# Kernel tuning notes

Measured on AMD Instinct MI355X. Metric: run time of the kernel, lower is better.

Reference implementation:

```python
import jax, jax.numpy as jnp
import numpy as np

B, N, C = 4, 1024, 1024
H = 16
HD = C // H
FF = 4 * C
EPS = 1e-6


def layernorm(x, g, b):
    mu = jnp.mean(x, axis=-1, keepdims=True)
    var = jnp.mean((x - mu) ** 2, axis=-1, keepdims=True)
    return (x - mu) * jax.lax.rsqrt(var + EPS) * g + b


def setup_inputs() -> dict:
    key = jax.random.key(0)
    ks = jax.random.split(key, 16)
    s = lambda fan_in: 1.0 / np.sqrt(fan_in)
    inp = {
        "x": jax.random.normal(ks[0], (B, N, C), dtype=jnp.float32),
        "qkv_w": jax.random.normal(ks[1], (3 * C, C), dtype=jnp.float32) * s(C),
        "qkv_b": jnp.zeros((3 * C,), jnp.float32),
        "attn_proj_w": jax.random.normal(ks[2], (C, C), dtype=jnp.float32) * s(C),
        "attn_proj_b": jnp.zeros((C,), jnp.float32),
        "blk_proj_w": jax.random.normal(ks[3], (C, C), dtype=jnp.float32) * s(C),
        "blk_proj_b": jnp.zeros((C,), jnp.float32),
        "ln1_g": jnp.ones((C,), jnp.float32),
        "ln1_b": jnp.zeros((C,), jnp.float32),
        "ln2_g": jnp.ones((C,), jnp.float32),
        "ln2_b": jnp.zeros((C,), jnp.float32),
        "fc1_w": jax.random.normal(ks[4], (FF, C), dtype=jnp.float32) * s(C),
        "fc1_b": jnp.zeros((FF,), jnp.float32),
        "fc2_w": jax.random.normal(ks[5], (C, FF), dtype=jnp.float32) * s(FF),
        "fc2_b": jnp.zeros((C,), jnp.float32),
        "mask": jnp.ones((B, N), jnp.int32),  # unused by the original forward
    }
    return inp


def reference(x, qkv_w, qkv_b, attn_proj_w, attn_proj_b, blk_proj_w, blk_proj_b,
              ln1_g, ln1_b, ln2_g, ln2_b, fc1_w, fc1_b, fc2_w, fc2_b, mask):
    shortcut = x
    xn = layernorm(x, ln1_g, ln1_b)

    # QKV projection: [B,N,3C] -> [3,B,H,N,HD]
    qkv = xn @ qkv_w.T + qkv_b
    qkv = qkv.reshape(B, N, 3, H, HD).transpose(2, 0, 3, 1, 4)
    q, k, v = qkv[0], qkv[1], qkv[2]
    scale = HD ** -0.5
    attn = jnp.einsum('bhqd,bhkd->bhqk', q * scale, k)
    attn = jax.nn.softmax(attn, axis=-1)
    o = jnp.einsum('bhqk,bhkd->bhqd', attn, v)
    o = o.transpose(0, 2, 1, 3).reshape(B, N, C)
    o = o @ attn_proj_w.T + attn_proj_b  # attention-internal proj

    x = shortcut + (o @ blk_proj_w.T + blk_proj_b)  # Block's extra proj + residual

    h = layernorm(x, ln2_g, ln2_b)
    h = jax.nn.gelu(h @ fc1_w.T + fc1_b, approximate=False)
    h = h @ fc2_w.T + fc2_b
    return x + h
```

## Files before the change

### kernel.cpp

```cpp
#include <hip/hip_runtime.h>

typedef unsigned short u16;
typedef __attribute__((ext_vector_type(8))) short short8;
typedef __attribute__((ext_vector_type(4))) float f32x4;

#define DEVI __device__ __forceinline__

static constexpr int Nn = 1024;
static constexpr int Cc = 1024;

DEVI u16 f2bf(float f) {
  union { float f; unsigned u; } v; v.f = f;
  unsigned r = v.u + 0x7fffu + ((v.u >> 16) & 1u);
  return (u16)(r >> 16);
}

DEVI void async_ld16(const void* g, void* lds) {
  __builtin_amdgcn_global_load_lds(
      (__attribute__((address_space(1))) void*)g,
      (__attribute__((address_space(3))) void*)lds, 16, 0, 0);
}

__global__ __launch_bounds__(256) void cvt_all(
    const float* __restrict__ s0, const float* __restrict__ s2,
    const float* __restrict__ s3, const float* __restrict__ s4,
    u16* __restrict__ out) {
  const size_t j = ((size_t)blockIdx.x * 256 + threadIdx.x) * 4;
  size_t i; const float* src; size_t lo;
  if (j < 3145728) { i = j; src = s0; lo = 0; }
  else {
    i = j + 1048576;
    if (i < 5242880)      { src = s2; lo = 4194304; }
    else if (i < 9437184) { src = s3; lo = 5242880; }
    else                  { src = s4; lo = 9437184; }
  }
  const float4 v = *(const float4*)&src[i - lo];
  ushort4 o;
  o.x = f2bf(v.x); o.y = f2bf(v.y); o.z = f2bf(v.z); o.w = f2bf(v.w);
  *(ushort4*)&out[i] = o;
}

__global__ __launch_bounds__(256) void transpose_wT(const float* __restrict__ in,
                                                    u16* __restrict__ out) {
  __shared__ u16 tile[64][72];
  const int bx = blockIdx.x & 15, by = blockIdx.x >> 4;
  const int tr = threadIdx.x >> 2;
  const int tc4 = (threadIdx.x & 3) * 16;
#pragma unroll
  for (int j = 0; j < 4; ++j) {
    const float4 v = *(const float4*)&in[(size_t)(by * 64 + tr) * 1024 +
                                         bx * 64 + tc4 + j * 4];
    tile[tc4 + j * 4 + 0][tr] = f2bf(v.x);
    tile[tc4 + j * 4 + 1][tr] = f2bf(v.y);
    tile[tc4 + j * 4 + 2][tr] = f2bf(v.z);
    tile[tc4 + j * 4 + 3][tr] = f2bf(v.w);
  }
  __syncthreads();
#pragma unroll
  for (int j = 0; j < 4; ++j) {
    ushort4 o;
    o.x = tile[tr][tc4 + j * 4 + 0];
    o.y = tile[tr][tc4 + j * 4 + 1];
    o.z = tile[tr][tc4 + j * 4 + 2];
    o.w = tile[tr][tc4 + j * 4 + 3];
    *(ushort4*)&out[(size_t)(bx * 64 + tr) * 1024 + by * 64 + tc4 + j * 4] = o;
  }
}

__global__ __launch_bounds__(256) void cbias_k(const float* __restrict__ apb,
                                               const float* __restrict__ bpw,
                                               const float* __restrict__ bpb,
                                               float* __restrict__ cb) {
  const int j = blockIdx.x * 4 + (threadIdx.x >> 6);
  const int lane = threadIdx.x & 63;
  float s = 0.f;
  for (int k = lane; k < 1024; k += 64) s += apb[k] * bpw[(size_t)j * 1024 + k];
#pragma unroll
  for (int m = 1; m < 64; m <<= 1) s += __shfl_xor(s, m);
  if (lane == 0) cb[j] = s + bpb[j];
}

__global__ __launch_bounds__(256) void gemm64(const u16* __restrict__ A,
                                              const u16* __restrict__ W,
                                              u16* __restrict__ out, int K) {
  __shared__ __align__(16) u16 As[64 * 64];
  __shared__ __align__(16) u16 Bs[64 * 64];
  const int tid = threadIdx.x;
  const int wave = tid >> 6, lane = tid & 63;
  const int g = lane >> 4, lr = lane & 15;
  const int brow = (blockIdx.x >> 4) << 6, bcol = (blockIdx.x & 15) << 6;
  const int srow = lane >> 3;
  const int scg = (lane & 7) ^ srow;
  const int swz = (lr & 7) << 4;

  f32x4 acc[4];
#pragma unroll
  for (int j = 0; j < 4; ++j) acc[j] = (f32x4){0.f, 0.f, 0.f, 0.f};

  for (int k0 = 0; k0 < K; k0 += 64) {
#pragma unroll
    for (int u = 0; u < 2; ++u) {
      async_ld16(A + (size_t)(brow + u * 32 + wave * 8 + srow) * K + k0 + scg * 8,
                 (char*)As + u * 4096 + wave * 1024);
      async_ld16(W + (size_t)(bcol + u * 32 + wave * 8 + srow) * K + k0 + scg * 8,
                 (char*)Bs + u * 4096 + wave * 1024);
    }
    __syncthreads();
    short8 af[2], bf[4][2];
#pragma unroll
    for (int kk = 0; kk < 2; ++kk)
      af[kk] = *(const short8*)((char*)As + (wave * 16 + lr) * 128 +
                                ((kk * 64 + g * 16) ^ swz));
#pragma unroll
    for (int nf = 0; nf < 4; ++nf)
#pragma unroll
      for (int kk = 0; kk < 2; ++kk)
        bf[nf][kk] = *(const short8*)((char*)Bs + (nf * 16 + lr) * 128 +
                                      ((kk * 64 + g * 16) ^ swz));
#pragma unroll
    for (int kk = 0; kk < 2; ++kk)
#pragma unroll
      for (int nf = 0; nf < 4; ++nf)
        acc[nf] = __builtin_amdgcn_mfma_f32_16x16x32_bf16(af[kk], bf[nf][kk],
                                                          acc[nf], 0, 0, 0);
    __syncthreads();
  }
#pragma unroll
  for (int nf = 0; nf < 4; ++nf)
#pragma unroll
    for (int reg = 0; reg < 4; ++reg)
      out[(size_t)(brow + wave * 16 + g * 4 + reg) * 1024 +
          bcol + nf * 16 + lr] = f2bf(acc[nf][reg]);
}

__global__ __launch_bounds__(256) void vtrans(const u16* __restrict__ qkv,
                                              u16* __restrict__ vt) {
  __shared__ u16 tile[64][72];
  const int bh = blockIdx.x >> 4, tb = blockIdx.x & 15;
  const int b = bh >> 4, h = bh & 15;
  const int t0 = tb * 64;
  const int tid = threadIdx.x;
  const int rr = tid >> 3, c8 = (tid & 7) * 8;
#pragma unroll
  for (int r = 0; r < 2; ++r) {
    const int t = r * 32 + rr;
    const short8 v = *(const short8*)(qkv + (size_t)(b * Nn + t0 + t) * 3072 +
                                      2048 + h * 64 + c8);
#pragma unroll
    for (int j = 0; j < 8; ++j) tile[t][c8 + j] = (u16)v[j];
  }
  __syncthreads();
#pragma unroll
  for (int r = 0; r < 2; ++r) {
    const int d = r * 32 + rr;
    short8 o;
#pragma unroll
    for (int j = 0; j < 8; ++j) o[j] = (short)tile[c8 + j][d];
    *(short8*)(vt + (size_t)(bh * 64 + d) * 1024 + t0 + c8) = o;
  }
}

__global__ __launch_bounds__(256) void ln_bf16(const float* __restrict__ x,
                                               const float* __restrict__ gg,
                                               const float* __restrict__ bb,
                                               u16* __restrict__ out) {
  const int row = blockIdx.x;
  const float4 v = ((const float4*)(x + (size_t)row * 1024))[threadIdx.x];
  float s  = v.x + v.y + v.z + v.w;
  float s2 = v.x * v.x + v.y * v.y + v.z * v.z + v.w * v.w;
#pragma unroll
  for (int m = 1; m < 64; m <<= 1) { s += __shfl_xor(s, m); s2 += __shfl_xor(s2, m); }
  __shared__ float ps[4], ps2[4];
  const int wave = threadIdx.x >> 6;
  if ((threadIdx.x & 63) == 0) { ps[wave] = s; ps2[wave] = s2; }
  __syncthreads();
  s = ps[0] + ps[1] + ps[2] + ps[3];
  s2 = ps2[0] + ps2[1] + ps2[2] + ps2[3];
  const float mu = s * (1.0f / 1024.0f);
  const float var = s2 * (1.0f / 1024.0f) - mu * mu;
  const float rs = rsqrtf(var + 1e-6f);
  const float4 gv = ((const float4*)gg)[threadIdx.x];
  const float4 bv = ((const float4*)bb)[threadIdx.x];
  ushort4 o;
  o.x = f2bf((v.x - mu) * rs * gv.x + bv.x);
  o.y = f2bf((v.y - mu) * rs * gv.y + bv.y);
  o.z = f2bf((v.z - mu) * rs * gv.z + bv.z);
  o.w = f2bf((v.w - mu) * rs * gv.w + bv.w);
  ((ushort4*)(out + (size_t)row * 1024))[threadIdx.x] = o;
}

template <bool GELU_, bool OUTBF>
__global__ __launch_bounds__(512, 4) void gemmS(
    const u16* __restrict__ A, const u16* __restrict__ W,
    const float* __restrict__ bias, void* __restrict__ out,
    int M, int N, int K) {
  __shared__ __align__(16) u16 As[256 * 64];
  __shared__ __align__(16) u16 Bs[128 * 64];
  const int tid = threadIdx.x;
  const int wave = tid >> 6, lane = tid & 63;
  const int g = lane >> 4, lr = lane & 15;
  const int wm = wave >> 1, wn = wave & 1;
  const int ntile = N >> 7;
  const int nwg = gridDim.x;
  int bid = blockIdx.x;
  bid = (bid & 7) * (nwg >> 3) + (bid >> 3);
  const int brow = (bid / ntile) << 8, bcol = (bid % ntile) << 7;

  const int sru = wave * 8 + (lane >> 3);
  const int scg = (lane & 7) ^ (lane >> 3);
  const int swz = (lr & 7) << 4;

  f32x4 acc[4][4];
#pragma unroll
  for (int i = 0; i < 4; ++i)
#pragma unroll
    for (int j = 0; j < 4; ++j) acc[i][j] = (f32x4){0.f, 0.f, 0.f, 0.f};

  for (int k0 = 0; k0 < K; k0 += 64) {
#pragma unroll
    for (int u = 0; u < 2; ++u)
      async_ld16(W + (size_t)(bcol + u * 64 + sru) * K + k0 + scg * 8,
                 (char*)Bs + u * 8192 + wave * 1024);
#pragma unroll
    for (int u = 0; u < 4; ++u)
      async_ld16(A + (size_t)(brow + u * 64 + sru) * K + k0 + scg * 8,
                 (char*)As + u * 8192 + wave * 1024);
    asm volatile("s_waitcnt vmcnt(0)" ::: "memory");
    __builtin_amdgcn_s_barrier();

    short8 bf[4][2];
#pragma unroll
    for (int nf = 0; nf < 4; ++nf) {
      const int row = wn * 64 + nf * 16 + lr;
#pragma unroll
      for (int kk = 0; kk < 2; ++kk)
        bf[nf][kk] = *(const short8*)((const char*)Bs + row * 128 +
                                      ((kk * 64 + g * 16) ^ swz));
    }
    __builtin_amdgcn_s_setprio(1);
#pragma unroll
    for (int mf = 0; mf < 4; ++mf) {
      short8 af[2];
      const int row = wm * 64 + mf * 16 + lr;
#pragma unroll
      for (int kk = 0; kk < 2; ++kk)
        af[kk] = *(const short8*)((const char*)As + row * 128 +
                                  ((kk * 64 + g * 16) ^ swz));
#pragma unroll
      for (int nf = 0; nf < 4; ++nf)
#pragma unroll
        for (int kk = 0; kk < 2; ++kk)
          acc[mf][nf] = __builtin_amdgcn_mfma_f32_16x16x32_bf16(
              af[kk], bf[nf][kk], acc[mf][nf], 0, 0, 0);
    }
    __builtin_amdgcn_s_setprio(0);
    __builtin_amdgcn_s_barrier();
  }

#pragma unroll
  for (int mf = 0; mf < 4; ++mf)
#pragma unroll
    for (int nf = 0; nf < 4; ++nf) {
      const int cI = bcol + wn * 64 + nf * 16 + lr;
      const float bv = bias[cI];
#pragma unroll
      for (int reg = 0; reg < 4; ++reg) {
        const int r = brow + wm * 64 + mf * 16 + g * 4 + reg;
        float v = acc[mf][nf][reg] + bv;
        if (GELU_) v = 0.5f * v * (1.0f + erff(v * 0.70710678118654752f));
        if (OUTBF) ((u16*)out)[(size_t)r * N + cI] = f2bf(v);
        else       ((float*)out)[(size_t)r * N + cI] = v;
      }
    }
}

template <bool RESID, bool OUTBF>
__global__ __launch_bounds__(512, 2) void gemm128t(
    const u16* __restrict__ A, const u16* __restrict__ W,
    const float* __restrict__ bias, const float* __restrict__ resid,
    void* __restrict__ out, int M, int N, int K) {
  __shared__ __align__(16) u16 smem[49152];
  const int tid = threadIdx.x;
  const int wave = tid >> 6, lane = tid & 63;
  const int g = lane >> 4, lr = lane & 15;
  const int kg = wave & 1, ws = wave >> 1;
  const int wm = ws >> 1, wn = ws & 1;
  const int ntile = N >> 7;
  const int nwg = gridDim.x;
  int bid = blockIdx.x;
  bid = (bid & 7) * (nwg >> 3) + (bid >> 3);
  const int brow = (bid / ntile) << 7, bcol = (bid % ntile) << 7;

  const int sru = wave * 8 + (lane >> 3);
  const int scg = (lane & 7) ^ (lane >> 3);
  const int NT = K >> 6;

  f32x4 acc[4][4];
#pragma unroll
  for (int i = 0; i < 4; ++i)
#pragma unroll
    for (int j = 0; j < 4; ++j) acc[i][j] = (f32x4){0.f, 0.f, 0.f, 0.f};

  auto STAGE = [&](int b, int kt) {
    char* base = (char*)smem + b * 32768;
#pragma unroll
    for (int u = 0; u < 2; ++u)
      async_ld16(W + (size_t)(bcol + u * 64 + sru) * K + (size_t)kt * 64 + scg * 8,
                 base + 16384 + u * 8192 + wave * 1024);
#pragma unroll
    for (int u = 0; u < 2; ++u)
      async_ld16(A + (size_t)(brow + u * 64 + sru) * K + (size_t)kt * 64 + scg * 8,
                 base + u * 8192 + wave * 1024);
  };

  const int colb = kg * 64 + g * 16;
  const int swz = (lr & 7) << 4;

  STAGE(0, 0);
  STAGE(1, 1 < NT ? 1 : 0);
  asm volatile("s_waitcnt vmcnt(4)" ::: "memory");
  __builtin_amdgcn_s_barrier();

  for (int t = 0; t < NT; ++t) {
    const int b = t % 3;
    const char* Ab = (const char*)smem + b * 32768;
    const char* Bb = Ab + 16384;

    short8 bf[4], af[4];
#pragma unroll
    for (int nf = 0; nf < 4; ++nf)
      bf[nf] = *(const short8*)(Bb + (wn * 64 + nf * 16 + lr) * 128 +
                                (colb ^ swz));
#pragma unroll
    for (int mf = 0; mf < 2; ++mf) {
      af[mf]     = *(const short8*)(Ab + (wm * 32 + mf * 16 + lr) * 128 +
                                    (colb ^ swz));
      af[mf + 2] = *(const short8*)(Ab + (64 + wm * 32 + mf * 16 + lr) * 128 +
                                    (colb ^ swz));
    }
    {
      const int pt = (t + 2 < NT) ? t + 2 : NT - 1;
      STAGE((t + 2) % 3, pt);
    }
    __builtin_amdgcn_s_setprio(1);
#pragma unroll
    for (int mf = 0; mf < 4; ++mf)
#pragma unroll
      for (int nf = 0; nf < 4; ++nf)
        acc[mf][nf] = __builtin_amdgcn_mfma_f32_16x16x32_bf16(
            af[mf], bf[nf], acc[mf][nf], 0, 0, 0);
    __builtin_amdgcn_s_setprio(0);
    asm volatile("s_waitcnt vmcnt(4)" ::: "memory");
    __builtin_amdgcn_s_barrier();
  }

  asm volatile("s_waitcnt vmcnt(0)" ::: "memory");
  __syncthreads();
  float* pr = (float*)smem + (size_t)((wm << 1) | wn) * 4096;
  if (kg == 1) {
#pragma unroll
    for (int mf = 0; mf < 4; ++mf)
#pragma unroll
      for (int nf = 0; nf < 4; ++nf)
#pragma unroll
        for (int reg = 0; reg < 4; ++reg) {
          const int lrow = mf * 16 + g * 4 + reg;
          const int w = lrow * 64 +
                        ((nf * 16 + lr) ^ (g << 2) ^ ((g & 1) << 4));
          pr[w] = acc[mf][nf][reg];
        }
  }
  __syncthreads();
  if (kg == 0) {
#pragma unroll
    for (int mf = 0; mf < 4; ++mf) {
      const int rb = brow + ((mf < 2) ? wm * 32 + mf * 16
                                      : 64 + wm * 32 + (mf - 2) * 16);
#pragma unroll
      for (int nf = 0; nf < 4; ++nf) {
        const int cI = bcol + wn * 64 + nf * 16 + lr;
        const float bv = bias[cI];
#pragma unroll
        for (int reg = 0; reg < 4; ++reg) {
          const int lrow = mf * 16 + g * 4 + reg;
          const int w = lrow * 64 +
                        ((nf * 16 + lr) ^ (g << 2) ^ ((g & 1) << 4));
          const int r = rb + g * 4 + reg;
          float v = acc[mf][nf][reg] + pr[w] + bv;
          if (RESID) v += resid[(size_t)r * N + cI];
          if (OUTBF) ((u16*)out)[(size_t)r * N + cI] = f2bf(v);
          else       ((float*)out)[(size_t)r * N + cI] = v;
        }
      }
    }
  }
}

__global__ __launch_bounds__(256) void attn_kernel(const u16* __restrict__ qkv,
                                                   const u16* __restrict__ vt,
                                                   u16* __restrict__ o_out) {
  const int D = blockIdx.x;
  const int bh = (D & 7) + 8 * (D >> 7);
  const int qb = (D >> 3) & 15;
  const int b = bh >> 4, h = bh & 15;
  const int tid = threadIdx.x, wave = tid >> 6, lane = tid & 63;
  const int g = lane >> 4, lr = lane & 15;
  const u16* qg = qkv + (size_t)b * Nn * 3072 + h * 64;
  const u16* kg = qg + 1024;
  const u16* vgt = vt + (size_t)bh * 64 * 1024;

  __shared__ __align__(16) u16 Kl[64 * 64];
  __shared__ __align__(16) u16 Vt[64 * 64];
  __shared__ __align__(16) u16 Pl[64 * 64];

  const int q0 = qb * 64 + wave * 16;
  short8 qf[2];
#pragma unroll
  for (int kf = 0; kf < 2; ++kf)
    qf[kf] = *(const short8*)(qg + (size_t)(q0 + lr) * 3072 + kf * 32 + g * 8);

  f32x4 o[4];
  float ll[4];
#pragma unroll
  for (int df = 0; df < 4; ++df) o[df] = (f32x4){0.f, 0.f, 0.f, 0.f};
#pragma unroll
  for (int r = 0; r < 4; ++r) ll[r] = 0.f;

  for (int t0 = 0; t0 < Nn; t0 += 64) {
#pragma unroll
    for (int r = 0; r < 2; ++r) {
      const int c = r * 256 + wave * 64 + lane;
      const int t = c >> 3;
      const int ob = ((c & 7) << 4) ^ ((t & 7) << 4);
      async_ld16(kg + (size_t)(t0 + t) * 3072 + (ob >> 1),
                 (char*)Kl + (size_t)(r * 256 + wave * 64) * 16);
      async_ld16(vgt + (size_t)t * 1024 + t0 + (ob >> 1),
                 (char*)Vt + (size_t)(r * 256 + wave * 64) * 16);
    }
    __syncthreads();

    short8 kfr[4][2];
#pragma unroll
    for (int tf = 0; tf < 4; ++tf) {
      const int t = tf * 16 + lr;
#pragma unroll
      for (int kf = 0; kf < 2; ++kf)
        kfr[tf][kf] = *(const short8*)((const char*)Kl + t * 128 +
                                       ((kf * 64 + g * 16) ^ ((t & 7) << 4)));
    }
    f32x4 s[4];
    __builtin_amdgcn_s_setprio(1);
#pragma unroll
    for (int tf = 0; tf < 4; ++tf) {
      f32x4 z = (f32x4){0.f, 0.f, 0.f, 0.f};
      z = __builtin_amdgcn_mfma_f32_16x16x32_bf16(qf[0], kfr[tf][0], z, 0, 0, 0);
      z = __builtin_amdgcn_mfma_f32_16x16x32_bf16(qf[1], kfr[tf][1], z, 0, 0, 0);
      s[tf] = z;
    }
    __builtin_amdgcn_s_setprio(0);

    short8 vfr[4][2];
#pragma unroll
    for (int df = 0; df < 4; ++df) {
      const int d = df * 16 + lr;
#pragma unroll
      for (int kf = 0; kf < 2; ++kf)
        vfr[df][kf] = *(const short8*)((const char*)Vt + d * 128 +
                                       ((kf * 64 + g * 16) ^ ((d & 7) << 4)));
    }

#pragma unroll
    for (int tf = 0; tf < 4; ++tf)
#pragma unroll
      for (int reg = 0; reg < 4; ++reg) {
        const float p = __expf(s[tf][reg] * 0.125f);
        s[tf][reg] = p;
        ll[reg] += p;
      }

#pragma unroll
    for (int tf = 0; tf < 4; ++tf)
#pragma unroll
      for (int reg = 0; reg < 4; ++reg) {
        const int m = wave * 16 + g * 4 + reg;
        const int t2 = (tf * 16 + lr) * 2;
        *(u16*)((char*)Pl + m * 128 + (t2 ^ ((m & 7) << 4))) = f2bf(s[tf][reg]);
      }
    short8 pa[2];
#pragma unroll
    for (int kf = 0; kf < 2; ++kf)
      pa[kf] = *(const short8*)((const char*)Pl + (wave * 16 + lr) * 128 +
                                ((kf * 64 + g * 16) ^ ((lr & 7) << 4)));
    __builtin_amdgcn_s_setprio(1);
#pragma unroll
    for (int df = 0; df < 4; ++df) {
      o[df] = __builtin_amdgcn_mfma_f32_16x16x32_bf16(pa[0], vfr[df][0], o[df], 0, 0, 0);
      o[df] = __builtin_amdgcn_mfma_f32_16x16x32_bf16(pa[1], vfr[df][1], o[df], 0, 0, 0);
    }
    __builtin_amdgcn_s_setprio(0);
    __syncthreads();
  }

#pragma unroll
  for (int reg = 0; reg < 4; ++reg) {
#pragma unroll
    for (int msk = 1; msk < 16; msk <<= 1) ll[reg] += __shfl_xor(ll[reg], msk);
    const float inv = 1.0f / ll[reg];
    const int row = b * Nn + qb * 64 + wave * 16 + g * 4 + reg;
#pragma unroll
    for (int df = 0; df < 4; ++df) {
      const int col = h * 64 + df * 16 + lr;
      o_out[(size_t)row * 1024 + col] = f2bf(o[df][reg] * inv);
    }
  }
}

extern "C" void kernel_launch(void* const* d_in, const int* in_sizes, int n_in,
                              void* d_out, int out_size, void* d_ws, size_t ws_size,
                              hipStream_t stream) {
  const float* x    = (const float*)d_in[0];
  const float* qkvw = (const float*)d_in[1];
  const float* qkvb = (const float*)d_in[2];
  const float* apw  = (const float*)d_in[3];
  const float* apb  = (const float*)d_in[4];
  const float* bpw  = (const float*)d_in[5];
  const float* bpb  = (const float*)d_in[6];
  const float* ln1g = (const float*)d_in[7];
  const float* ln1b = (const float*)d_in[8];
  const float* ln2g = (const float*)d_in[9];
  const float* ln2b = (const float*)d_in[10];
  const float* fc1w = (const float*)d_in[11];
  const float* fc1b = (const float*)d_in[12];
  const float* fc2w = (const float*)d_in[13];
  const float* fc2b = (const float*)d_in[14];
  float* out = (float*)d_out;

  char* ws = (char*)d_ws;
  size_t off = 0;
  auto alloc = [&](size_t bytes) {
    char* p = ws + off;
    off += (bytes + 255) & ~(size_t)255;
    return p;
  };
  u16* wqkv  = (u16*)alloc((size_t)3145728 * 2);
  u16* wap   = (u16*)alloc((size_t)1048576 * 2);
  u16* wbp   = (u16*)alloc((size_t)1048576 * 2);
  u16* wfc1  = (u16*)alloc((size_t)4194304 * 2);
  u16* wfc2  = (u16*)alloc((size_t)4194304 * 2);
  u16* xn    = (u16*)alloc((size_t)4194304 * 2);
  u16* qkvbf = (u16*)alloc((size_t)12582912 * 2);
  u16* obuf  = (u16*)alloc((size_t)4194304 * 2);
  float* x2  = (float*)alloc((size_t)4194304 * 4);
  u16* wapT  = (u16*)alloc((size_t)1048576 * 2);
  u16* wc    = (u16*)alloc((size_t)1048576 * 2);
  float* cb  = (float*)alloc(1024 * 4);
  u16* vt    = (u16*)alloc((size_t)4194304 * 2);
  u16* ff    = qkvbf;
  (void)wap;

  cvt_all<<<12288, 256, 0, stream>>>(qkvw, bpw, fc1w, fc2w, wqkv);
  transpose_wT<<<256, 256, 0, stream>>>(apw, wapT);
  cbias_k<<<256, 256, 0, stream>>>(apb, bpw, bpb, cb);

  gemm64<<<256, 256, 0, stream>>>(wbp, wapT, wc, 1024);

  ln_bf16<<<4096, 256, 0, stream>>>(x, ln1g, ln1b, xn);

  gemmS<false, true><<<384, 512, 0, stream>>>(
      xn, wqkv, qkvb, qkvbf, 4096, 3072, 1024);

  vtrans<<<1024, 256, 0, stream>>>(qkvbf, vt);

  attn_kernel<<<1024, 256, 0, stream>>>(qkvbf, vt, obuf);

  gemm128t<true, false><<<256, 512, 0, stream>>>(
      obuf, wc, cb, x, x2, 4096, 1024, 1024);

  ln_bf16<<<4096, 256, 0, stream>>>(x2, ln2g, ln2b, xn);

  gemmS<true, true><<<512, 512, 0, stream>>>(
      xn, wfc1, fc1b, ff, 4096, 4096, 1024);

  gemm128t<true, false><<<256, 512, 0, stream>>>(
      ff, wfc2, fc2b, x2, out, 4096, 1024, 4096);
}
```

Baseline: 226.5 us.

## Triple-buffer K/V tiles in attention kernel with async prefetch two ahead

The attention kernel now keeps three LDS buffers for K and V tiles and issues the async global-to-LDS loads two iterations ahead. A vmcnt wait plus a raw barrier replaces the per-iteration __syncthreads, so loads overlap with the MFMA and softmax work instead of stalling on each tile. A GELU template parameter is added to gemm128t but is disabled at every call site. The extra buffers raise LDS use per block, which may lower occupancy, and the hand-written waitcnt counts must match the number of outstanding loads.

```diff
diff --git a/kernel.cpp b/kernel.cpp
--- a/kernel.cpp
+++ b/kernel.cpp
@@ -274,7 +274,7 @@
     }
 }
 
-template <bool RESID, bool OUTBF>
+template <bool GELU_, bool RESID, bool OUTBF>
 __global__ __launch_bounds__(512, 2) void gemm128t(
     const u16* __restrict__ A, const u16* __restrict__ W,
     const float* __restrict__ bias, const float* __restrict__ resid,
@@ -387,6 +387,7 @@
                         ((nf * 16 + lr) ^ (g << 2) ^ ((g & 1) << 4));
           const int r = rb + g * 4 + reg;
           float v = acc[mf][nf][reg] + pr[w] + bv;
+          if (GELU_) v = 0.5f * v * (1.0f + erff(v * 0.70710678118654752f));
           if (RESID) v += resid[(size_t)r * N + cI];
           if (OUTBF) ((u16*)out)[(size_t)r * N + cI] = f2bf(v);
           else       ((float*)out)[(size_t)r * N + cI] = v;
@@ -409,8 +410,8 @@
   const u16* kg = qg + 1024;
   const u16* vgt = vt + (size_t)bh * 64 * 1024;
 
-  __shared__ __align__(16) u16 Kl[64 * 64];
-  __shared__ __align__(16) u16 Vt[64 * 64];
+  __shared__ __align__(16) u16 Kl[3][64 * 64];
+  __shared__ __align__(16) u16 Vl[3][64 * 64];
   __shared__ __align__(16) u16 Pl[64 * 64];
 
   const int q0 = qb * 64 + wave * 16;
@@ -426,18 +427,31 @@
 #pragma unroll
   for (int r = 0; r < 4; ++r) ll[r] = 0.f;
 
-  for (int t0 = 0; t0 < Nn; t0 += 64) {
+  auto stageKV = [&](int buf, int t0) {
 #pragma unroll
     for (int r = 0; r < 2; ++r) {
-      const int c = r * 256 + wave * 64 + lane;
-      const int t = c >> 3;
-      const int ob = ((c & 7) << 4) ^ ((t & 7) << 4);
-      async_ld16(kg + (size_t)(t0 + t) * 3072 + (ob >> 1),
-                 (char*)Kl + (size_t)(r * 256 + wave * 64) * 16);
-      async_ld16(vgt + (size_t)t * 1024 + t0 + (ob >> 1),
-                 (char*)Vt + (size_t)(r * 256 + wave * 64) * 16);
-    }
-    __syncthreads();
+      const int cc = r * 256 + wave * 64 + lane;
+      const int tt = cc >> 3;
+      const int ob = ((cc & 7) << 4) ^ ((tt & 7) << 4);
+      async_ld16(kg + (size_t)(t0 + tt) * 3072 + (ob >> 1),
+                 (char*)Kl[buf] + (size_t)(r * 256 + wave * 64) * 16);
+      async_ld16(vgt + (size_t)tt * 1024 + t0 + (ob >> 1),
+                 (char*)Vl[buf] + (size_t)(r * 256 + wave * 64) * 16);
+    }
+  };
+
+  const int NT = Nn / 64;
+  stageKV(0, 0);
+  stageKV(1, 64);
+  asm volatile("s_waitcnt vmcnt(4)" ::: "memory");
+  __builtin_amdgcn_s_barrier();
+
+  for (int ti = 0; ti < NT; ++ti) {
+    const int cb = ti % 3;
+    {
+      const int pt = (ti + 2 < NT) ? ti + 2 : NT - 1;
+      stageKV((ti + 2) % 3, pt * 64);
+    }
 
     short8 kfr[4][2];
 #pragma unroll
@@ -445,7 +459,7 @@
       const int t = tf * 16 + lr;
 #pragma unroll
       for (int kf = 0; kf < 2; ++kf)
-        kfr[tf][kf] = *(const short8*)((const char*)Kl + t * 128 +
+        kfr[tf][kf] = *(const short8*)((const char*)Kl[cb] + t * 128 +
                                        ((kf * 64 + g * 16) ^ ((t & 7) << 4)));
     }
     f32x4 s[4];
@@ -465,7 +479,7 @@
       const int d = df * 16 + lr;
 #pragma unroll
       for (int kf = 0; kf < 2; ++kf)
-        vfr[df][kf] = *(const short8*)((const char*)Vt + d * 128 +
+        vfr[df][kf] = *(const short8*)((const char*)Vl[cb] + d * 128 +
                                        ((kf * 64 + g * 16) ^ ((d & 7) << 4)));
     }
 
@@ -498,8 +512,11 @@
       o[df] = __builtin_amdgcn_mfma_f32_16x16x32_bf16(pa[1], vfr[df][1], o[df], 0, 0, 0);
     }
     __builtin_amdgcn_s_setprio(0);
-    __syncthreads();
-  }
+
+    asm volatile("s_waitcnt vmcnt(4)" ::: "memory");
+    __builtin_amdgcn_s_barrier();
+  }
+  asm volatile("s_waitcnt vmcnt(0)" ::: "memory");
 
 #pragma unroll
   for (int reg = 0; reg < 4; ++reg) {
@@ -573,7 +590,7 @@
 
   attn_kernel<<<1024, 256, 0, stream>>>(qkvbf, vt, obuf);
 
-  gemm128t<true, false><<<256, 512, 0, stream>>>(
+  gemm128t<false, true, false><<<256, 512, 0, stream>>>(
       obuf, wc, cb, x, x2, 4096, 1024, 1024);
 
   ln_bf16<<<4096, 256, 0, stream>>>(x2, ln2g, ln2b, xn);
@@ -581,6 +598,6 @@
   gemmS<true, true><<<512, 512, 0, stream>>>(
       xn, wfc1, fc1b, ff, 4096, 4096, 1024);
 
-  gemm128t<true, false><<<256, 512, 0, stream>>>(
+  gemm128t<false, true, false><<<256, 512, 0, stream>>>(
       ff, wfc2, fc2b, x2, out, 4096, 1024, 4096);
 }
```

Measured after the change: 234.8 us. 3.7% more time.
